# Performance work log

Measured on AMD Instinct MI355X. Metric: run time of the kernel, lower is better.

The kernel has to match this reference:

```python
import jax, jax.numpy as jnp
import numpy as np

IN_CH = 128
HID = 64
EPS = 1e-5
N_NODES = 20000
E_UND = 80000


def _build_line_graph(edge_index, num_nodes):
    # dedupe to unique undirected edges (src<dst); line-graph nodes = these edges
    src = np.asarray(edge_index[0]); dst = np.asarray(edge_index[1])
    m = src < dst
    u, v = src[m], dst[m]
    key = u.astype(np.int64) * num_nodes + v.astype(np.int64)
    _, first = np.unique(key, return_index=True)
    u, v = u[first], v[first]
    E = u.shape[0]
    # incidence lists grouped by node; all ordered pairs of co-incident edges
    nodes = np.concatenate([u, v])
    eids = np.concatenate([np.arange(E), np.arange(E)])
    order = np.argsort(nodes, kind="stable")
    nodes_s, eids_s = nodes[order], eids[order]
    counts = np.bincount(nodes_s, minlength=num_nodes)
    offsets = np.concatenate([np.zeros(1, np.int64), np.cumsum(counts)])
    grp_start = offsets[nodes_s]
    reps = counts[nodes_s]
    total = int(reps.sum())
    starts = np.cumsum(reps) - reps
    idx = np.arange(total) - np.repeat(starts, reps) + np.repeat(grp_start, reps)
    row = np.repeat(eids_s, reps); col = eids_s[idx]
    keep = row != col
    return np.stack([u, v]), np.stack([row[keep], col[keep]])


def _gcn_conv(x, src, dst, W, b):
    # PyG GCNConv: add self loops, symmetric D^-1/2 (A+I) D^-1/2 normalization
    N = x.shape[0]
    sl = jnp.arange(N)
    s = jnp.concatenate([src, sl]); d = jnp.concatenate([dst, sl])
    deg = jax.ops.segment_sum(jnp.ones(s.shape[0], x.dtype), d, num_segments=N)
    dinv = jax.lax.rsqrt(jnp.maximum(deg, 1.0))
    h = x @ W
    msg = h[s] * (dinv[s] * dinv[d])[:, None]
    return jax.ops.segment_sum(msg, d, num_segments=N) + b


def _edge_scores(line_x, lsrc, ldst, W1, b1, gamma1, beta1, W2, b2):
    h = _gcn_conv(line_x, lsrc, ldst, W1, b1)
    mu = h.mean(0); var = h.var(0)  # BatchNorm1d, training-mode batch stats
    h = jax.nn.relu(gamma1 * (h - mu) * jax.lax.rsqrt(var + EPS) + beta1)
    return jax.nn.sigmoid(_gcn_conv(h, lsrc, ldst, W2, b2))[:, 0]


def _cluster(clean, topk_idx, num_nodes):
    ti = np.asarray(topk_idx)
    sel_src = np.asarray(clean[0])[ti]; sel_dst = np.asarray(clean[1])[ti]
    n2c = np.arange(num_nodes)
    rev = sel_dst[::-1]
    _, fi = np.unique(rev, return_index=True)
    last = sel_dst.shape[0] - 1 - fi
    n2c[sel_dst[last]] = sel_src[last]
    uniq = np.unique(n2c)
    M = int(uniq.shape[0])
    old_to_new = np.full(num_nodes, -1, np.int64)
    old_to_new[uniq] = np.arange(M)
    return old_to_new[n2c], uniq, M


def _make_graph():
    rng = np.random.default_rng(0)
    a = rng.integers(0, N_NODES, E_UND)
    off = rng.integers(1, N_NODES, E_UND)
    b = (a + off) % N_NODES  # no self loops
    u = np.minimum(a, b); v = np.maximum(a, b)
    return np.stack([np.concatenate([u, v]), np.concatenate([v, u])]).astype(np.int64)


def _make_params():
    ks = jax.random.split(jax.random.key(0), 4)
    x = jax.random.normal(ks[0], (N_NODES, IN_CH), jnp.float32)
    W1 = jax.random.normal(ks[1], (IN_CH, HID), jnp.float32) / np.float32(np.sqrt(IN_CH))
    b1 = jnp.zeros((HID,), jnp.float32)
    gamma1 = jnp.ones((HID,), jnp.float32)
    beta1 = jnp.zeros((HID,), jnp.float32)
    W2 = jax.random.normal(ks[2], (HID, 1), jnp.float32) / np.float32(np.sqrt(HID))
    b2 = jnp.zeros((1,), jnp.float32)
    return x, W1, b1, gamma1, beta1, W2, b2


def setup_inputs() -> dict:
    x, W1, b1, gamma1, beta1, W2, b2 = _make_params()
    return {
        "x": x, "W1": W1, "b1": b1, "gamma1": gamma1, "beta1": beta1,
        "W2": W2, "b2": b2,
        "edge_index": jnp.asarray(_make_graph()),
        "batch": jnp.zeros((N_NODES,), jnp.int32),
    }


def reference(x, W1, b1, gamma1, beta1, W2, b2, edge_index, batch):
    N = x.shape[0]
    clean, line_ei = _build_line_graph(edge_index, N)
    csrc = jnp.asarray(clean[0]); cdst = jnp.asarray(clean[1])
    lsrc = jnp.asarray(line_ei[0]); ldst = jnp.asarray(line_ei[1])
    line_x = 0.5 * (x[csrc] + x[cdst])  # line-graph node features
    scores = _edge_scores(line_x, lsrc, ldst, W1, b1, gamma1, beta1, W2, b2)
    E_c = scores.shape[0]
    k = max(1, min(E_c // 2, N // 2))
    _, topk_idx = jax.lax.top_k(scores, k)
    new_indices, uniq, M = _cluster(clean, topk_idx, N)
    ni = jnp.asarray(new_indices)
    # aggregate: per-cluster mean of member node features (code's weights are unused)
    counts = jax.ops.segment_sum(jnp.ones(N, x.dtype), ni, num_segments=M)
    x_pool = jax.ops.segment_sum(x, ni, num_segments=M) / counts[:, None]
    batch_pool = batch[jnp.asarray(uniq)]
    # build_new_edges: relabel, drop self loops, coalesce (sorted unique)
    ei = np.asarray(edge_index)
    ns = new_indices[ei[0]]; nd = new_indices[ei[1]]
    keep = ns != nd
    pk = ns[keep] * M + nd[keep]
    upk = np.unique(pk)
    edge_index_pool = jnp.asarray(np.stack([upk // M, upk % M]))
    return (x_pool, edge_index_pool, batch_pool, scores, ni)
```

## Files before the change

### kernel.cpp

```cpp
#include <hip/hip_runtime.h>
#include <stdint.h>

typedef unsigned long long u64;
typedef unsigned int u32;

#define NND 20000
#define EUA 160000
#define EFE 80000
#define ICH 128
#define HIDC 64
#define SCAN_BS 256
#define NB_N ((NND + 255) / 256)
#define NB_EU ((EUA + 255) / 256)
#define NB_EF ((EFE + 255) / 256)
#define NB_E64 ((EFE * HIDC + 255) / 256)
#define NB_X ((NND * ICH + 255) / 256)
#define NSCAN_B ((NND + SCAN_BS - 1) / SCAN_BS)
#define HIST_BLOCKS 128
#define GEB 64
#define XS_PAD 132
#define NCHAIN 4096
#define OUT_MAX_INIT 3000000
#define SEL_BINS 1024


__global__ void scan1(const int* __restrict__ in, int* __restrict__ out,
                      int* __restrict__ bsums, int n) {
    __shared__ int sh[SCAN_BS];
    int tid = threadIdx.x;
    int i = blockIdx.x * SCAN_BS + tid;
    int v = (i < n) ? in[i] : 0;
    sh[tid] = v;
    __syncthreads();
    for (int o = 1; o < SCAN_BS; o <<= 1) {
        int t = (tid >= o) ? sh[tid - o] : 0;
        __syncthreads();
        sh[tid] += t;
        __syncthreads();
    }
    if (i < n) out[i] = sh[tid] - v;
    if (tid == SCAN_BS - 1) bsums[blockIdx.x] = sh[tid];
}
__global__ void scan2(int* __restrict__ bsums, int nb) {
    __shared__ int sh[160];
    int tid = threadIdx.x;
    if (tid < nb) sh[tid] = bsums[tid];
    __syncthreads();
    if (tid == 0) {
        int acc = 0;
        for (int i = 0; i < nb; i++) { int t = sh[i]; sh[i] = acc; acc += t; }
        sh[nb] = acc;
    }
    __syncthreads();
    if (tid <= nb) bsums[tid] = sh[tid];
}
__global__ void scan3(int* __restrict__ out, const int* __restrict__ bsums,
                      int n, int nb, int* __restrict__ totalDst) {
    int i = blockIdx.x * SCAN_BS + threadIdx.x;
    if (i < n) out[i] += bsums[blockIdx.x];
    if (i == 0) {
        int tot = bsums[nb];
        out[n] = tot;
        *totalDst = tot;
    }
}

__global__ void kFilterCount(const int* __restrict__ ei, int* __restrict__ cnt) {
    int i = blockIdx.x * 256 + threadIdx.x;
    if (i >= EUA) return;
    int s = ei[i], d = ei[EUA + i];
    if (s < d) atomicAdd(&cnt[s], 1);
}
__global__ void kFilterScatter(const int* __restrict__ ei, const int* __restrict__ offA,
                               int* __restrict__ tmp, int* __restrict__ bucketV) {
    int i = blockIdx.x * 256 + threadIdx.x;
    if (i >= EUA) return;
    int s = ei[i], d = ei[EUA + i];
    if (s < d) {
        int p = offA[s] + atomicAdd(&tmp[s], 1);
        bucketV[p] = d;
    }
}
__global__ void kRankSort(const int* __restrict__ in, int* __restrict__ out,
                          const int* __restrict__ offA, int* __restrict__ ucnt) {
    int a = blockIdx.x;
    int s = offA[a], e = offA[a + 1], len = e - s;
    for (int j = threadIdx.x; j < len; j += 64) {
        int v = in[s + j];
        int r = 0;
        for (int i = 0; i < len; i++) {
            int w = in[s + i];
            r += (w < v) || (w == v && i < j);
        }
        out[s + r] = v;
    }
    __syncthreads();
    int c = 0;
    for (int j = threadIdx.x; j < len; j += 64)
        c += (j == 0) || (out[s + j] != out[s + j - 1]);
#pragma unroll
    for (int o = 32; o > 0; o >>= 1) c += __shfl_down(c, o, 64);
    if (threadIdx.x == 0) ucnt[a] = c;
}
__global__ void kCompactInc(const int* __restrict__ arr, const int* __restrict__ offA,
                            const int* __restrict__ uoff, int* __restrict__ eU,
                            int* __restrict__ eV, int* __restrict__ icnt) {
    int u = blockIdx.x * 256 + threadIdx.x;
    if (u >= NND) return;
    int s = offA[u], e = offA[u + 1], o = uoff[u];
    int myc = 0;
    for (int i = s; i < e; i++)
        if (i == s || arr[i] != arr[i - 1]) {
            int v = arr[i];
            eU[o] = u; eV[o] = v; o++;
            atomicAdd(&icnt[v], 1);
            myc++;
        }
    if (myc) atomicAdd(&icnt[u], myc);
}

__global__ void kIncScatterDinv(const int* __restrict__ eU, const int* __restrict__ eV,
                                const int* __restrict__ scal, const int* __restrict__ ioff,
                                int* __restrict__ itmp, int* __restrict__ ilist,
                                const int* __restrict__ icnt, float* __restrict__ dinv) {
    int e = blockIdx.x * 256 + threadIdx.x;
    if (e >= scal[0]) return;
    int u = eU[e], v = eV[e];
    ilist[ioff[u] + atomicAdd(&itmp[u], 1)] = e;
    ilist[ioff[v] + atomicAdd(&itmp[v], 1)] = e;
    dinv[e] = rsqrtf((float)(icnt[u] + icnt[v] - 1));
}

__global__ void kGemm(const float* __restrict__ x, const float* __restrict__ W1,
                      const int* __restrict__ eU, const int* __restrict__ eV,
                      const int* __restrict__ scal, float* __restrict__ h) {
    __shared__ float W1s[ICH][HIDC];
    __shared__ float xs[GEB][XS_PAD];
    int t = threadIdx.x;
    int E = scal[0];
    int e0 = blockIdx.x * GEB;
    if (e0 >= E) return;

    {
        const float4* Wv = (const float4*)W1;
        float4* Ws = (float4*)&W1s[0][0];
        for (int i = t; i < ICH * HIDC / 4; i += 256) Ws[i] = Wv[i];
    }
    {
        int eb = t >> 2, q = t & 3;
        int e = e0 + eb;
        if (e < E) {
            int u = eU[e], v = eV[e];
            const float4* xu = (const float4*)(x + (size_t)u * ICH) + q * 8;
            const float4* xv = (const float4*)(x + (size_t)v * ICH) + q * 8;
            float* xd = &xs[eb][q * 32];
#pragma unroll
            for (int i = 0; i < 8; i++) {
                float4 a = xu[i], b = xv[i];
                xd[i * 4 + 0] = 0.5f * (a.x + b.x);
                xd[i * 4 + 1] = 0.5f * (a.y + b.y);
                xd[i * 4 + 2] = 0.5f * (a.z + b.z);
                xd[i * 4 + 3] = 0.5f * (a.w + b.w);
            }
        }
    }
    __syncthreads();

    int cg4 = (t & 15) * 4;
    int es = t >> 4;
    float a00=0,a01=0,a02=0,a03=0, a10=0,a11=0,a12=0,a13=0;
    float a20=0,a21=0,a22=0,a23=0, a30=0,a31=0,a32=0,a33=0;
#pragma unroll 4
    for (int k = 0; k < ICH; k++) {
        float4 wv = *(const float4*)&W1s[k][cg4];
        float x0 = xs[es][k], x1 = xs[es + 16][k];
        float x2 = xs[es + 32][k], x3 = xs[es + 48][k];
        a00 += x0 * wv.x; a01 += x0 * wv.y; a02 += x0 * wv.z; a03 += x0 * wv.w;
        a10 += x1 * wv.x; a11 += x1 * wv.y; a12 += x1 * wv.z; a13 += x1 * wv.w;
        a20 += x2 * wv.x; a21 += x2 * wv.y; a22 += x2 * wv.z; a23 += x2 * wv.w;
        a30 += x3 * wv.x; a31 += x3 * wv.y; a32 += x3 * wv.z; a33 += x3 * wv.w;
    }
    int e;
    e = e0 + es;
    if (e < E) *(float4*)&h[(size_t)e * HIDC + cg4] = make_float4(a00, a01, a02, a03);
    e = e0 + es + 16;
    if (e < E) *(float4*)&h[(size_t)e * HIDC + cg4] = make_float4(a10, a11, a12, a13);
    e = e0 + es + 32;
    if (e < E) *(float4*)&h[(size_t)e * HIDC + cg4] = make_float4(a20, a21, a22, a23);
    e = e0 + es + 48;
    if (e < E) *(float4*)&h[(size_t)e * HIDC + cg4] = make_float4(a30, a31, a32, a33);
}

__global__ void kSGather(const float* __restrict__ h, const float* __restrict__ dinv,
                         const int* __restrict__ ioff, const int* __restrict__ ilist,
                         float* __restrict__ S) {
    int n = blockIdx.x;
    int c = threadIdx.x;
    int s = ioff[n], e = ioff[n + 1];
    float acc = 0.f;
    for (int j = s; j < e; j++) {
        int ed = ilist[j];
        acc += h[(size_t)ed * HIDC + c] * dinv[ed];
    }
    S[(size_t)n * HIDC + c] = acc;
}
__global__ void kConv1(const float* __restrict__ h, const float* __restrict__ S,
                       const float* __restrict__ dinv, const int* __restrict__ eU,
                       const int* __restrict__ eV, const float* __restrict__ b1,
                       const int* __restrict__ scal, float* __restrict__ h2) {
    int idx = blockIdx.x * 256 + threadIdx.x;
    int e = idx >> 6;
    if (e >= scal[0]) return;
    int c = idx & 63;
    float a = dinv[e];
    h2[idx] = a * (S[(size_t)eU[e] * HIDC + c] + S[(size_t)eV[e] * HIDC + c]) -
              a * a * h[idx] + b1[c];
}

__global__ void kRed1(const float* __restrict__ h2, const int* __restrict__ scal,
                      const float* __restrict__ muvar, float* __restrict__ partial,
                      int pass) {
    int t = threadIdx.x;
    int g = blockIdx.x * 4 + (t >> 6);
    int c = t & 63;
    int E = scal[0];
    float m = pass ? muvar[c] : 0.f;
    float acc = 0.f;
    for (int e = g; e < E; e += NCHAIN) {
        float v = h2[(size_t)e * HIDC + c];
        if (pass) { float d = v - m; acc += d * d; }
        else acc += v;
    }
    partial[g * HIDC + c] = acc;
}
__global__ void kRed2(const float* __restrict__ partial, const int* __restrict__ scal,
                      float* __restrict__ muvar, int pass) {
    __shared__ float sh[4][HIDC];
    int t = threadIdx.x;
    int q = t >> 6, c = t & 63;
    float acc = 0.f;
    int g0 = q * (NCHAIN / 4);
    for (int g = g0; g < g0 + NCHAIN / 4; g++) acc += partial[g * HIDC + c];
    sh[q][c] = acc;
    __syncthreads();
    if (q == 0) {
        float s = ((sh[0][c] + sh[1][c]) + sh[2][c]) + sh[3][c];
        muvar[pass * HIDC + c] = s / (float)scal[0];
    }
}
__global__ void kNormZ(const float* __restrict__ h2, const float* __restrict__ muvar,
                       const float* __restrict__ gamma1, const float* __restrict__ beta1,
                       const float* __restrict__ W2, const int* __restrict__ scal,
                       float* __restrict__ z) {
    int idx = blockIdx.x * 256 + threadIdx.x;
    int e = idx >> 6;
    if (e >= scal[0]) return;
    int c = idx & 63;
    float t = gamma1[c] * (h2[idx] - muvar[c]) * rsqrtf(muvar[HIDC + c] + 1e-5f) + beta1[c];
    t = t > 0.f ? t : 0.f;
    float p = t * W2[c];
#pragma unroll
    for (int o = 32; o > 0; o >>= 1) p += __shfl_down(p, o, 64);
    if (c == 0) z[e] = p;
}
__global__ void kS2(const float* __restrict__ z, const float* __restrict__ dinv,
                    const int* __restrict__ ioff, const int* __restrict__ ilist,
                    float* __restrict__ S2) {
    int n = blockIdx.x * 256 + threadIdx.x;
    if (n >= NND) return;
    float acc = 0.f;
    for (int j = ioff[n]; j < ioff[n + 1]; j++) {
        int e = ilist[j];
        acc += z[e] * dinv[e];
    }
    S2[n] = acc;
}
__global__ void kScore(const float* __restrict__ z, const float* __restrict__ S2,
                       const float* __restrict__ dinv, const int* __restrict__ eU,
                       const int* __restrict__ eV, const float* __restrict__ b2,
                       const int* __restrict__ scal, float* __restrict__ score,
                       u64* __restrict__ okey, int* __restrict__ krem,
                       u64* __restrict__ pref) {
    int e = blockIdx.x * 256 + threadIdx.x;
    int E = scal[0];
    if (e >= E) return;
    if (e == 0) {
        int k = E / 2;
        if (k > NND / 2) k = NND / 2;
        if (k < 1) k = 1;
        *krem = k;
        *pref = 0ULL;
    }
    float a = dinv[e];
    float l = a * (S2[eU[e]] + S2[eV[e]]) - a * a * z[e] + b2[0];
    float s = 1.f / (1.f + expf(-l));
    score[e] = s;
    u32 b = __float_as_uint(s);
    b = (b >> 31) ? ~b : (b | 0x80000000u);
    okey[e] = (((u64)b) << 17) | (u32)(0x1FFFFu - (u32)e);
}

__global__ void kHist(const u64* __restrict__ okey, const int* __restrict__ scal,
                      int* __restrict__ hist, const u64* __restrict__ pref,
                      u64 maskHi, int shift) {
    __shared__ int sh[4][SEL_BINS];
    int t = threadIdx.x;
    for (int j = t; j < 4 * SEL_BINS; j += 256) ((int*)sh)[j] = 0;
    __syncthreads();
    int wv = t >> 6;
    int E = scal[0];
    u64 p = *pref;
    for (int e = blockIdx.x * 256 + t; e < E; e += HIST_BLOCKS * 256) {
        u64 kk = okey[e];
        if ((kk & maskHi) == p)
            atomicAdd(&sh[wv][(int)((kk >> shift) & (SEL_BINS - 1))], 1);
    }
    __syncthreads();
    for (int j = t; j < SEL_BINS; j += 256) {
        int v = sh[0][j] + sh[1][j] + sh[2][j] + sh[3][j];
        if (v) atomicAdd(&hist[j], v);
    }
}
__global__ void kSelPass(int* __restrict__ hist, u64* __restrict__ pref,
                         int* __restrict__ krem, int shift) {
    __shared__ int sh[SEL_BINS];
    __shared__ int aux[256];
    __shared__ int shKr;
    int t = threadIdx.x;
    int g = 0;
#pragma unroll
    for (int j = 0; j < 4; j++) {
        int v = hist[4 * t + j];
        sh[4 * t + j] = v;
        hist[4 * t + j] = 0;
        g += v;
    }
    if (t == 0) shKr = *krem;
    aux[t] = g;
    __syncthreads();
    for (int o = 1; o < 256; o <<= 1) {
        int v = (t + o < 256) ? aux[t + o] : 0;
        __syncthreads();
        aux[t] += v;
        __syncthreads();
    }
    int kr = shKr;
    int suf = aux[t] - g;
    if (suf < kr && kr <= suf + g) {
        int cum = suf, found = 4 * t;
        for (int b = 4 * t + 3; b >= 4 * t; b--) {
            int hc = sh[b];
            if (cum + hc >= kr) { found = b; break; }
            cum += hc;
        }
        *krem = kr - cum;
        *pref |= ((u64)found) << shift;
    }
}

__global__ void kMinKeyInit(const u64* __restrict__ okey, const int* __restrict__ eV,
                            const int* __restrict__ scal, const u64* __restrict__ pref,
                            u64* __restrict__ minOkey, int* __restrict__ n2c) {
    int i = blockIdx.x * 256 + threadIdx.x;
    if (i < NND) n2c[i] = i;
    if (i < scal[0]) {
        u64 k = okey[i];
        if (k >= *pref) atomicMin(&minOkey[eV[i]], k);
    }
}
__global__ void kN2cSet(const u64* __restrict__ okey, const int* __restrict__ eU,
                        const int* __restrict__ eV, const int* __restrict__ scal,
                        const u64* __restrict__ pref, const u64* __restrict__ minOkey,
                        int* __restrict__ n2c) {
    int e = blockIdx.x * 256 + threadIdx.x;
    if (e >= scal[0]) return;
    u64 k = okey[e];
    int v = eV[e];
    if (k >= *pref && k == minOkey[v]) n2c[v] = eU[e];
}
__global__ void kPresent(const int* __restrict__ n2c, int* __restrict__ present) {
    int n = blockIdx.x * 256 + threadIdx.x;
    if (n < NND) present[n2c[n]] = 1;
}
__global__ void kNiCcnt(const int* __restrict__ n2c, const int* __restrict__ o2n,
                        int* __restrict__ ni, int* __restrict__ ccnt) {
    int n = blockIdx.x * 256 + threadIdx.x;
    if (n >= NND) return;
    int m = o2n[n2c[n]];
    ni[n] = m;
    atomicAdd(&ccnt[m], 1);
}

__global__ void kXacc(const float* __restrict__ x, const int* __restrict__ ni,
                      float* __restrict__ dout) {
    int idx = blockIdx.x * 256 + threadIdx.x;
    if (idx >= NND * ICH) return;
    int n = idx >> 7, c = idx & 127;
    atomicAdd(&dout[(size_t)ni[n] * ICH + c], x[idx]);
}
__global__ void kXdiv(float* __restrict__ dout, const int* __restrict__ ccnt,
                      const int* __restrict__ scal) {
    int idx = blockIdx.x * 256 + threadIdx.x;
    int m = idx >> 7;
    if (m >= scal[2]) return;
    dout[idx] /= (float)ccnt[m];
}

__global__ void kCEcount(const int* __restrict__ ei, const int* __restrict__ ni,
                         int* __restrict__ ecnt2) {
    int i = blockIdx.x * 256 + threadIdx.x;
    if (i >= EUA) return;
    int a = ni[ei[i]], b = ni[ei[EUA + i]];
    if (a != b) atomicAdd(&ecnt2[a], 1);
}
__global__ void kCEscatter(const int* __restrict__ ei, const int* __restrict__ ni,
                           const int* __restrict__ eoff2, int* __restrict__ etmp2,
                           int* __restrict__ bkD) {
    int i = blockIdx.x * 256 + threadIdx.x;
    if (i >= EUA) return;
    int a = ni[ei[i]], b = ni[ei[EUA + i]];
    if (a != b) {
        int p = eoff2[a] + atomicAdd(&etmp2[a], 1);
        bkD[p] = b;
    }
}
__global__ void kCEwrite(const int* __restrict__ bkD2, const int* __restrict__ offA,
                         const int* __restrict__ ueoff, const int* __restrict__ scal,
                         float* __restrict__ dout) {
    int a = blockIdx.x * 256 + threadIdx.x;
    if (a >= NND) return;
    int s = offA[a], e = offA[a + 1];
    int M = scal[2], Ep = scal[3];
    float* r0 = dout + (size_t)M * ICH;
    float* r1 = r0 + Ep;
    int o = ueoff[a];
    for (int i = s; i < e; i++)
        if (i == s || bkD2[i] != bkD2[i - 1]) {
            r0[o] = (float)a;
            r1[o] = (float)bkD2[i];
            o++;
        }
}

__global__ void kTail(const int* __restrict__ batch, const int* __restrict__ present,
                      const int* __restrict__ o2n, const float* __restrict__ score,
                      const int* __restrict__ ni, const int* __restrict__ scal,
                      float* __restrict__ dout) {
    int i = blockIdx.x * 256 + threadIdx.x;
    int E = scal[0], M = scal[2], Ep = scal[3];
    size_t base = (size_t)M * ICH + 2 * (size_t)Ep;
    if (i < NND && present[i]) dout[base + o2n[i]] = (float)batch[i];
    if (i < E) dout[base + M + i] = score[i];
    if (i < NND) dout[base + M + E + i] = (float)ni[i];
}

extern "C" void kernel_launch(void* const* d_in, const int* in_sizes, int n_in,
                              void* d_out, int out_size, void* d_ws, size_t ws_size,
                              hipStream_t stream) {
    (void)in_sizes; (void)n_in; (void)ws_size;
    const float* x = (const float*)d_in[0];
    const float* W1 = (const float*)d_in[1];
    const float* b1 = (const float*)d_in[2];
    const float* gamma1 = (const float*)d_in[3];
    const float* beta1 = (const float*)d_in[4];
    const float* W2 = (const float*)d_in[5];
    const float* b2 = (const float*)d_in[6];
    const int* ei = (const int*)d_in[7];
    const int* batch = (const int*)d_in[8];
    float* dout = (float*)d_out;

    char* w = (char*)d_ws;
    size_t off = 0;
    auto carve = [&](size_t bytes) -> void* {
        off = (off + 255) & ~(size_t)255;
        void* p = w + off;
        off += bytes;
        return p;
    };
    char* zero0 = w;
    int* cnt = (int*)carve(NND * 4);
    int* tmp = (int*)carve(NND * 4);
    int* icnt = (int*)carve(NND * 4);
    int* itmp = (int*)carve(NND * 4);
    int* present = (int*)carve(NND * 4);
    int* ccnt = (int*)carve(NND * 4);
    int* ecnt2 = (int*)carve(NND * 4);
    int* etmp2 = (int*)carve(NND * 4);
    int* scal = (int*)carve(16 * 4);
    int* hist = (int*)carve(SEL_BINS * 4);
    size_t zeroBytes = off;
    int* offA = (int*)carve((NND + 2) * 4);
    int* ucnt = (int*)carve(NND * 4);
    int* uoff = (int*)carve((NND + 2) * 4);
    int* ioff = (int*)carve((NND + 2) * 4);
    int* bsums = (int*)carve((NSCAN_B + 2) * 4);
    int* n2c = (int*)carve(NND * 4);
    int* o2n = (int*)carve((NND + 2) * 4);
    int* niArr = (int*)carve(NND * 4);
    int* eoff2 = (int*)carve((NND + 2) * 4);
    int* uecnt = (int*)carve(NND * 4);
    int* ueoff = (int*)carve((NND + 2) * 4);
    int* bucketV = (int*)carve(EUA * 4);
    int* bucketS = (int*)carve(EUA * 4);
    int* eU = (int*)carve(EFE * 4);
    int* eV = (int*)carve(EFE * 4);
    int* ilist = (int*)carve(2 * EFE * 4);
    int* ilistS = (int*)carve(2 * EFE * 4);
    int* bkD = (int*)carve(EUA * 4);
    int* bkD2 = (int*)carve(EUA * 4);
    u64* okey = (u64*)carve(EFE * 8);
    u64* minOkey = (u64*)carve(NND * 8);
    u64* dpref = (u64*)carve(8);
    float* dinv = (float*)carve(EFE * 4);
    float* h = (float*)carve((size_t)EFE * HIDC * 4);
    float* h2 = (float*)carve((size_t)EFE * HIDC * 4);
    float* Snode = (float*)carve((size_t)NND * HIDC * 4);
    float* partial = (float*)carve((size_t)NCHAIN * HIDC * 4);
    float* muvar = (float*)carve(128 * 4);
    float* zArr = (float*)carve(EFE * 4);
    float* S2 = (float*)carve(NND * 4);
    float* score = (float*)carve(EFE * 4);

    auto scan = [&](const int* in, int* outp, int* totalDst) {
        scan1<<<NSCAN_B, SCAN_BS, 0, stream>>>(in, outp, bsums, NND);
        scan2<<<1, 128, 0, stream>>>(bsums, NSCAN_B);
        scan3<<<NSCAN_B, SCAN_BS, 0, stream>>>(outp, bsums, NND, NSCAN_B, totalDst);
    };

    size_t outInit = (size_t)out_size;
    if (outInit > OUT_MAX_INIT) outInit = OUT_MAX_INIT;
    hipMemsetAsync(zero0, 0, zeroBytes, stream);
    hipMemsetAsync(minOkey, 0xFF, NND * 8, stream);
    hipMemsetAsync(d_out, 0, outInit * 4, stream);

    kFilterCount<<<NB_EU, 256, 0, stream>>>(ei, cnt);
    scan(cnt, offA, scal + 15);
    kFilterScatter<<<NB_EU, 256, 0, stream>>>(ei, offA, tmp, bucketV);
    kRankSort<<<NND, 64, 0, stream>>>(bucketV, bucketS, offA, ucnt);
    scan(ucnt, uoff, scal + 0);
    kCompactInc<<<NB_N, 256, 0, stream>>>(bucketS, offA, uoff, eU, eV, icnt);

    scan(icnt, ioff, scal + 15);
    kIncScatterDinv<<<NB_EF, 256, 0, stream>>>(eU, eV, scal, ioff, itmp, ilist, icnt, dinv);
    kRankSort<<<NND, 64, 0, stream>>>(ilist, ilistS, ioff, tmp);

    kGemm<<<(EFE + GEB - 1) / GEB, 256, 0, stream>>>(x, W1, eU, eV, scal, h);
    kSGather<<<NND, HIDC, 0, stream>>>(h, dinv, ioff, ilistS, Snode);
    kConv1<<<NB_E64, 256, 0, stream>>>(h, Snode, dinv, eU, eV, b1, scal, h2);

    kRed1<<<NCHAIN / 4, 256, 0, stream>>>(h2, scal, muvar, partial, 0);
    kRed2<<<1, 256, 0, stream>>>(partial, scal, muvar, 0);
    kRed1<<<NCHAIN / 4, 256, 0, stream>>>(h2, scal, muvar, partial, 1);
    kRed2<<<1, 256, 0, stream>>>(partial, scal, muvar, 1);
    kNormZ<<<NB_E64, 256, 0, stream>>>(h2, muvar, gamma1, beta1, W2, scal, zArr);

    kS2<<<NB_N, 256, 0, stream>>>(zArr, dinv, ioff, ilistS, S2);
    kScore<<<NB_EF, 256, 0, stream>>>(zArr, S2, dinv, eU, eV, b2, scal, score, okey,
                                      scal + 1, dpref);

    for (int p = 0; p < 5; p++) {
        int shift = 40 - 10 * p;
        u64 maskHi = (~0ULL) << (shift + 10);
        kHist<<<HIST_BLOCKS, 256, 0, stream>>>(okey, scal, hist, dpref, maskHi, shift);
        kSelPass<<<1, 256, 0, stream>>>(hist, dpref, scal + 1, shift);
    }

    kMinKeyInit<<<NB_EF, 256, 0, stream>>>(okey, eV, scal, dpref, minOkey, n2c);
    kN2cSet<<<NB_EF, 256, 0, stream>>>(okey, eU, eV, scal, dpref, minOkey, n2c);
    kPresent<<<NB_N, 256, 0, stream>>>(n2c, present);
    scan(present, o2n, scal + 2);
    kNiCcnt<<<NB_N, 256, 0, stream>>>(n2c, o2n, niArr, ccnt);

    kXacc<<<NB_X, 256, 0, stream>>>(x, niArr, dout);
    kXdiv<<<NB_X, 256, 0, stream>>>(dout, ccnt, scal);

    kCEcount<<<NB_EU, 256, 0, stream>>>(ei, niArr, ecnt2);
    scan(ecnt2, eoff2, scal + 4);
    kCEscatter<<<NB_EU, 256, 0, stream>>>(ei, niArr, eoff2, etmp2, bkD);
    kRankSort<<<NND, 64, 0, stream>>>(bkD, bkD2, eoff2, uecnt);
    scan(uecnt, ueoff, scal + 3);
    kCEwrite<<<NB_N, 256, 0, stream>>>(bkD2, eoff2, ueoff, scal, dout);

    kTail<<<NB_EF, 256, 0, stream>>>(batch, present, o2n, score, niArr, scal, dout);
}
```

Baseline: 424.1 us.

## Fuse small kernels and widen radix-select bins to cut launch count

Merges the three-kernel scan into two by having each block re-scan the block sums. It also fuses the conv1 output with the first BatchNorm mean reduction, and folds the minOkey initialisation into the score kernel. The ni/cluster-count computation is fused into the feature accumulation, and the coarsened-edge write is fused with the tail outputs. Top-k radix selection now uses 4096 bins over four passes instead of 1024 bins over five, with the prefix seeded for the always-set top key bit. The aim is to remove launch and pass overhead, at the cost of redundant block-sum scans, a strided conv1 access pattern, and larger shared histograms.

```diff
diff --git a/kernel.cpp b/kernel.cpp
--- a/kernel.cpp
+++ b/kernel.cpp
@@ -21,11 +21,11 @@
 #define XS_PAD 132
 #define NCHAIN 4096
 #define OUT_MAX_INIT 3000000
-#define SEL_BINS 1024
-
-
-__global__ void scan1(const int* __restrict__ in, int* __restrict__ out,
-                      int* __restrict__ bsums, int n) {
+#define SEL_BINS 4096
+
+
+__global__ void kScanA(const int* __restrict__ in, int* __restrict__ out,
+                       int* __restrict__ bsums, int n) {
     __shared__ int sh[SCAN_BS];
     int tid = threadIdx.x;
     int i = blockIdx.x * SCAN_BS + tid;
@@ -41,10 +41,11 @@
     if (i < n) out[i] = sh[tid] - v;
     if (tid == SCAN_BS - 1) bsums[blockIdx.x] = sh[tid];
 }
-__global__ void scan2(int* __restrict__ bsums, int nb) {
+__global__ void kScanB(int* __restrict__ out, const int* __restrict__ bsums,
+                       int n, int nb, int* __restrict__ totalDst) {
     __shared__ int sh[160];
     int tid = threadIdx.x;
-    if (tid < nb) sh[tid] = bsums[tid];
+    if (tid <= nb) sh[tid] = (tid < nb) ? bsums[tid] : 0;
     __syncthreads();
     if (tid == 0) {
         int acc = 0;
@@ -52,14 +53,10 @@
         sh[nb] = acc;
     }
     __syncthreads();
-    if (tid <= nb) bsums[tid] = sh[tid];
-}
-__global__ void scan3(int* __restrict__ out, const int* __restrict__ bsums,
-                      int n, int nb, int* __restrict__ totalDst) {
-    int i = blockIdx.x * SCAN_BS + threadIdx.x;
-    if (i < n) out[i] += bsums[blockIdx.x];
+    int i = blockIdx.x * SCAN_BS + tid;
+    if (i < n) out[i] += sh[blockIdx.x];
     if (i == 0) {
-        int tot = bsums[nb];
+        int tot = sh[nb];
         out[n] = tot;
         *totalDst = tot;
     }
@@ -204,32 +201,37 @@
     }
     S[(size_t)n * HIDC + c] = acc;
 }
-__global__ void kConv1(const float* __restrict__ h, const float* __restrict__ S,
-                       const float* __restrict__ dinv, const int* __restrict__ eU,
-                       const int* __restrict__ eV, const float* __restrict__ b1,
-                       const int* __restrict__ scal, float* __restrict__ h2) {
-    int idx = blockIdx.x * 256 + threadIdx.x;
-    int e = idx >> 6;
-    if (e >= scal[0]) return;
-    int c = idx & 63;
-    float a = dinv[e];
-    h2[idx] = a * (S[(size_t)eU[e] * HIDC + c] + S[(size_t)eV[e] * HIDC + c]) -
-              a * a * h[idx] + b1[c];
-}
-
-__global__ void kRed1(const float* __restrict__ h2, const int* __restrict__ scal,
-                      const float* __restrict__ muvar, float* __restrict__ partial,
-                      int pass) {
+__global__ void kConv1Red1(const float* __restrict__ h, const float* __restrict__ S,
+                           const float* __restrict__ dinv, const int* __restrict__ eU,
+                           const int* __restrict__ eV, const float* __restrict__ b1,
+                           const int* __restrict__ scal, float* __restrict__ h2,
+                           float* __restrict__ partial) {
     int t = threadIdx.x;
     int g = blockIdx.x * 4 + (t >> 6);
     int c = t & 63;
     int E = scal[0];
-    float m = pass ? muvar[c] : 0.f;
+    float bc = b1[c];
     float acc = 0.f;
     for (int e = g; e < E; e += NCHAIN) {
-        float v = h2[(size_t)e * HIDC + c];
-        if (pass) { float d = v - m; acc += d * d; }
-        else acc += v;
+        float a = dinv[e];
+        float v = a * (S[(size_t)eU[e] * HIDC + c] + S[(size_t)eV[e] * HIDC + c]) -
+                  a * a * h[(size_t)e * HIDC + c] + bc;
+        h2[(size_t)e * HIDC + c] = v;
+        acc += v;
+    }
+    partial[g * HIDC + c] = acc;
+}
+__global__ void kRed1v(const float* __restrict__ h2, const int* __restrict__ scal,
+                       const float* __restrict__ muvar, float* __restrict__ partial) {
+    int t = threadIdx.x;
+    int g = blockIdx.x * 4 + (t >> 6);
+    int c = t & 63;
+    int E = scal[0];
+    float m = muvar[c];
+    float acc = 0.f;
+    for (int e = g; e < E; e += NCHAIN) {
+        float d = h2[(size_t)e * HIDC + c] - m;
+        acc += d * d;
     }
     partial[g * HIDC + c] = acc;
 }
@@ -280,8 +282,9 @@
                        const int* __restrict__ eV, const float* __restrict__ b2,
                        const int* __restrict__ scal, float* __restrict__ score,
                        u64* __restrict__ okey, int* __restrict__ krem,
-                       u64* __restrict__ pref) {
+                       u64* __restrict__ pref, u64* __restrict__ minOkey) {
     int e = blockIdx.x * 256 + threadIdx.x;
+    if (e < NND) minOkey[e] = ~0ULL;
     int E = scal[0];
     if (e >= E) return;
     if (e == 0) {
@@ -289,7 +292,7 @@
         if (k > NND / 2) k = NND / 2;
         if (k < 1) k = 1;
         *krem = k;
-        *pref = 0ULL;
+        *pref = 1ULL << 48;
     }
     float a = dinv[e];
     float l = a * (S2[eU[e]] + S2[eV[e]]) - a * a * z[e] + b2[0];
@@ -329,10 +332,10 @@
     int t = threadIdx.x;
     int g = 0;
 #pragma unroll
-    for (int j = 0; j < 4; j++) {
-        int v = hist[4 * t + j];
-        sh[4 * t + j] = v;
-        hist[4 * t + j] = 0;
+    for (int j = 0; j < 16; j++) {
+        int v = hist[16 * t + j];
+        sh[16 * t + j] = v;
+        hist[16 * t + j] = 0;
         g += v;
     }
     if (t == 0) shKr = *krem;
@@ -347,8 +350,8 @@
     int kr = shKr;
     int suf = aux[t] - g;
     if (suf < kr && kr <= suf + g) {
-        int cum = suf, found = 4 * t;
-        for (int b = 4 * t + 3; b >= 4 * t; b--) {
+        int cum = suf, found = 16 * t;
+        for (int b = 16 * t + 15; b >= 16 * t; b--) {
             int hc = sh[b];
             if (cum + hc >= kr) { found = b; break; }
             cum += hc;
@@ -382,21 +385,19 @@
     int n = blockIdx.x * 256 + threadIdx.x;
     if (n < NND) present[n2c[n]] = 1;
 }
-__global__ void kNiCcnt(const int* __restrict__ n2c, const int* __restrict__ o2n,
-                        int* __restrict__ ni, int* __restrict__ ccnt) {
-    int n = blockIdx.x * 256 + threadIdx.x;
-    if (n >= NND) return;
-    int m = o2n[n2c[n]];
-    ni[n] = m;
-    atomicAdd(&ccnt[m], 1);
-}
-
-__global__ void kXacc(const float* __restrict__ x, const int* __restrict__ ni,
-                      float* __restrict__ dout) {
+
+__global__ void kNiXacc(const float* __restrict__ x, const int* __restrict__ n2c,
+                        const int* __restrict__ o2n, int* __restrict__ ni,
+                        int* __restrict__ ccnt, float* __restrict__ dout) {
     int idx = blockIdx.x * 256 + threadIdx.x;
     if (idx >= NND * ICH) return;
     int n = idx >> 7, c = idx & 127;
-    atomicAdd(&dout[(size_t)ni[n] * ICH + c], x[idx]);
+    int m = o2n[n2c[n]];
+    atomicAdd(&dout[(size_t)m * ICH + c], x[idx]);
+    if (c == 0) {
+        ni[n] = m;
+        atomicAdd(&ccnt[m], 1);
+    }
 }
 __global__ void kXdiv(float* __restrict__ dout, const int* __restrict__ ccnt,
                       const int* __restrict__ scal) {
@@ -424,34 +425,30 @@
         bkD[p] = b;
     }
 }
-__global__ void kCEwrite(const int* __restrict__ bkD2, const int* __restrict__ offA,
-                         const int* __restrict__ ueoff, const int* __restrict__ scal,
-                         float* __restrict__ dout) {
-    int a = blockIdx.x * 256 + threadIdx.x;
-    if (a >= NND) return;
-    int s = offA[a], e = offA[a + 1];
-    int M = scal[2], Ep = scal[3];
-    float* r0 = dout + (size_t)M * ICH;
-    float* r1 = r0 + Ep;
-    int o = ueoff[a];
-    for (int i = s; i < e; i++)
-        if (i == s || bkD2[i] != bkD2[i - 1]) {
-            r0[o] = (float)a;
-            r1[o] = (float)bkD2[i];
-            o++;
-        }
-}
-
-__global__ void kTail(const int* __restrict__ batch, const int* __restrict__ present,
-                      const int* __restrict__ o2n, const float* __restrict__ score,
-                      const int* __restrict__ ni, const int* __restrict__ scal,
-                      float* __restrict__ dout) {
+__global__ void kCEwriteTail(const int* __restrict__ bkD2, const int* __restrict__ eoff2,
+                             const int* __restrict__ ueoff, const int* __restrict__ scal,
+                             const int* __restrict__ batch, const int* __restrict__ present,
+                             const int* __restrict__ o2n, const float* __restrict__ score,
+                             const int* __restrict__ ni, float* __restrict__ dout) {
     int i = blockIdx.x * 256 + threadIdx.x;
     int E = scal[0], M = scal[2], Ep = scal[3];
-    size_t base = (size_t)M * ICH + 2 * (size_t)Ep;
-    if (i < NND && present[i]) dout[base + o2n[i]] = (float)batch[i];
-    if (i < E) dout[base + M + i] = score[i];
-    if (i < NND) dout[base + M + E + i] = (float)ni[i];
+    size_t base = (size_t)M * ICH;
+    if (i < NND) {
+        int s = eoff2[i], e = eoff2[i + 1];
+        float* r0 = dout + base;
+        float* r1 = r0 + Ep;
+        int o = ueoff[i];
+        for (int j = s; j < e; j++)
+            if (j == s || bkD2[j] != bkD2[j - 1]) {
+                r0[o] = (float)i;
+                r1[o] = (float)bkD2[j];
+                o++;
+            }
+    }
+    size_t tb = base + 2 * (size_t)Ep;
+    if (i < NND && present[i]) dout[tb + o2n[i]] = (float)batch[i];
+    if (i < E) dout[tb + M + i] = score[i];
+    if (i < NND) dout[tb + M + E + i] = (float)ni[i];
 }
 
 extern "C" void kernel_launch(void* const* d_in, const int* in_sizes, int n_in,
@@ -522,15 +519,13 @@
     float* score = (float*)carve(EFE * 4);
 
     auto scan = [&](const int* in, int* outp, int* totalDst) {
-        scan1<<<NSCAN_B, SCAN_BS, 0, stream>>>(in, outp, bsums, NND);
-        scan2<<<1, 128, 0, stream>>>(bsums, NSCAN_B);
-        scan3<<<NSCAN_B, SCAN_BS, 0, stream>>>(outp, bsums, NND, NSCAN_B, totalDst);
+        kScanA<<<NSCAN_B, SCAN_BS, 0, stream>>>(in, outp, bsums, NND);
+        kScanB<<<NSCAN_B, SCAN_BS, 0, stream>>>(outp, bsums, NND, NSCAN_B, totalDst);
     };
 
     size_t outInit = (size_t)out_size;
     if (outInit > OUT_MAX_INIT) outInit = OUT_MAX_INIT;
     hipMemsetAsync(zero0, 0, zeroBytes, stream);
-    hipMemsetAsync(minOkey, 0xFF, NND * 8, stream);
     hipMemsetAsync(d_out, 0, outInit * 4, stream);
 
     kFilterCount<<<NB_EU, 256, 0, stream>>>(ei, cnt);
@@ -546,21 +541,19 @@
 
     kGemm<<<(EFE + GEB - 1) / GEB, 256, 0, stream>>>(x, W1, eU, eV, scal, h);
     kSGather<<<NND, HIDC, 0, stream>>>(h, dinv, ioff, ilistS, Snode);
-    kConv1<<<NB_E64, 256, 0, stream>>>(h, Snode, dinv, eU, eV, b1, scal, h2);
-
-    kRed1<<<NCHAIN / 4, 256, 0, stream>>>(h2, scal, muvar, partial, 0);
+    kConv1Red1<<<NCHAIN / 4, 256, 0, stream>>>(h, Snode, dinv, eU, eV, b1, scal, h2, partial);
     kRed2<<<1, 256, 0, stream>>>(partial, scal, muvar, 0);
-    kRed1<<<NCHAIN / 4, 256, 0, stream>>>(h2, scal, muvar, partial, 1);
+    kRed1v<<<NCHAIN / 4, 256, 0, stream>>>(h2, scal, muvar, partial);
     kRed2<<<1, 256, 0, stream>>>(partial, scal, muvar, 1);
     kNormZ<<<NB_E64, 256, 0, stream>>>(h2, muvar, gamma1, beta1, W2, scal, zArr);
 
     kS2<<<NB_N, 256, 0, stream>>>(zArr, dinv, ioff, ilistS, S2);
     kScore<<<NB_EF, 256, 0, stream>>>(zArr, S2, dinv, eU, eV, b2, scal, score, okey,
-                                      scal + 1, dpref);
-
-    for (int p = 0; p < 5; p++) {
-        int shift = 40 - 10 * p;
-        u64 maskHi = (~0ULL) << (shift + 10);
+                                      scal + 1, dpref, minOkey);
+
+    for (int p = 0; p < 4; p++) {
+        int shift = 36 - 12 * p;
+        u64 maskHi = (~0ULL) << (shift + 12);
         kHist<<<HIST_BLOCKS, 256, 0, stream>>>(okey, scal, hist, dpref, maskHi, shift);
         kSelPass<<<1, 256, 0, stream>>>(hist, dpref, scal + 1, shift);
     }
@@ -569,9 +562,7 @@
     kN2cSet<<<NB_EF, 256, 0, stream>>>(okey, eU, eV, scal, dpref, minOkey, n2c);
     kPresent<<<NB_N, 256, 0, stream>>>(n2c, present);
     scan(present, o2n, scal + 2);
-    kNiCcnt<<<NB_N, 256, 0, stream>>>(n2c, o2n, niArr, ccnt);
-
-    kXacc<<<NB_X, 256, 0, stream>>>(x, niArr, dout);
+    kNiXacc<<<NB_X, 256, 0, stream>>>(x, n2c, o2n, niArr, ccnt, dout);
     kXdiv<<<NB_X, 256, 0, stream>>>(dout, ccnt, scal);
 
     kCEcount<<<NB_EU, 256, 0, stream>>>(ei, niArr, ecnt2);
@@ -579,7 +570,6 @@
     kCEscatter<<<NB_EU, 256, 0, stream>>>(ei, niArr, eoff2, etmp2, bkD);
     kRankSort<<<NND, 64, 0, stream>>>(bkD, bkD2, eoff2, uecnt);
     scan(uecnt, ueoff, scal + 3);
-    kCEwrite<<<NB_N, 256, 0, stream>>>(bkD2, eoff2, ueoff, scal, dout);
-
-    kTail<<<NB_EF, 256, 0, stream>>>(batch, present, o2n, score, niArr, scal, dout);
-}
+    kCEwriteTail<<<NB_EF, 256, 0, stream>>>(bkD2, eoff2, ueoff, scal, batch, present,
+                                            o2n, score, niArr, dout);
+}
```

After: 412.6 us. -2.7%, faster.
